# Kernel tuning notes

Hardware: AMD Instinct MI355X
Metric: run time of the kernel (lower is better)

Reference implementation:

```python
import jax, jax.numpy as jnp
import numpy as np

B, L, C, H, W = 8, 8, 64, 56, 56
K = 3
EPS = 1e-5


def setup_inputs() -> dict:
    key = jax.random.key(0)
    ks = jax.random.split(key, 7)
    s = lambda k, shape, sc=0.05: jax.random.normal(k, shape, dtype=jnp.float32) * sc
    return {
        "x": jax.random.normal(ks[0], (B, L, C, H, W), dtype=jnp.float32),
        "temporal_w": s(ks[1], (C, C)),        # Conv3d 1x1x1 C->C
        "temporal_b": s(ks[2], (C,)),
        "fc_w": s(ks[3], (C,)),                # Conv3d 1x1x1 C->1
        "fc_b": s(ks[4], (1,)),
        "conv_w": s(ks[5], (C, C, K, K), 0.1), # self.weight [1,1,Co,Ci,k,k] core
        "conv_b": s(ks[6], (C,)),              # self.bias [1,1,Co] core
        "bn_gamma": jnp.ones((C,), jnp.float32),
        "bn_beta": jnp.zeros((C,), jnp.float32),
    }


def reference(x, temporal_w, temporal_b, fc_w, fc_b, conv_w, conv_b, bn_gamma, bn_beta):
    b, l, c, h, w = x.shape
    # ---- generateweight_fourier ----
    xin = jnp.transpose(x, (0, 2, 1, 3, 4))                # [B,C,L,H,W]
    f = jnp.fft.fft2(xin, axes=(3, 4), norm='ortho')       # spatial FFT
    f = jnp.fft.fft(f, axis=2, norm='ortho')               # temporal FFT
    allxin = xin + 0.01 * jnp.abs(f) * xin                 # Fourier2 attention + residual
    pooled = allxin.mean(axis=(3, 4))                      # AdaptiveAvgPool3d((None,1,1)) -> [B,C,L]
    # temporalconv: 1x1x1 Conv3d C->C on [B,C,L,1,1]
    calib = jnp.einsum('oc,bcl->bol', temporal_w, pooled) + temporal_b[None, :, None]  # [B,C,L]
    # fc: 1x1x1 Conv3d C->1
    fcout = jnp.einsum('c,bcl->bl', fc_w, pooled) + fc_b[0]                            # [B,L]
    # finalweight: weight[1,1,Co,Ci,k,k] * (calib+1) broadcast over Ci -> [B,L,Co,Ci,k,k]
    calib_blc = jnp.transpose(calib, (0, 2, 1)) + 1.0      # [B,L,Ci]
    fw = conv_w[None, None] * calib_blc[:, :, None, :, None, None]
    fb = conv_b[None, None, :] * (fcout + 1.0)[:, :, None] # [B,L,Co]
    # ---- dynamic per-(sample,frame) conv2d (groups = b*l) ----
    x_flat = x.reshape(b * l, c, h, w)
    fw_flat = fw.reshape(b * l, c, c, K, K)
    fb_flat = fb.reshape(b * l, c)

    def per_sample(xi, wi):
        return jax.lax.conv_general_dilated(
            xi[None], wi, window_strides=(1, 1), padding=[(1, 1), (1, 1)],
            dimension_numbers=('NCHW', 'OIHW', 'NCHW'))[0]

    out = jax.vmap(per_sample)(x_flat, fw_flat) + fb_flat[:, :, None, None]
    out = x_flat + out                                     # residual (gate=False)
    # BatchNorm2d (training-mode batch statistics)
    mean = out.mean(axis=(0, 2, 3), keepdims=True)
    var = out.var(axis=(0, 2, 3), keepdims=True)
    out = (out - mean) * jax.lax.rsqrt(var + EPS)
    out = out * bn_gamma[None, :, None, None] + bn_beta[None, :, None, None]
    out = out * jax.nn.sigmoid(out)                        # SiLU
    return out.reshape(b, l, c, h, w)
```

## Files before the change

kernel.cpp:

```cpp
#include <hip/hip_runtime.h>
#include <cmath>

#define HW 3136
#define NF 64
#define NBLK2 448

typedef __attribute__((ext_vector_type(8))) short short8;
typedef __attribute__((ext_vector_type(4))) float float4a;

__device__ __forceinline__ unsigned short f2bf(float f) {
    unsigned int u = __float_as_uint(f);
    u += 0x7fffu + ((u >> 16) & 1u);
    return (unsigned short)(u >> 16);
}
__device__ __forceinline__ float bf2f(unsigned short u) {
    return __uint_as_float(((unsigned int)u) << 16);
}

__global__ __launch_bounds__(256)
void pack_kernel(const float* __restrict__ cw,
                 unsigned short* __restrict__ Ffix,
                 unsigned short* __restrict__ Wp) {
    if (blockIdx.x < 64) {
        int idx = blockIdx.x * 256 + threadIdx.x;
        int j    = idx & 7;
        int lane = (idx >> 3) & 63;
        int ks   = (idx >> 9) & 3;
        int t    = (idx >> 11) & 3;
        int p    = (idx >> 13) & 1;
        int mn = t * 16 + (lane & 15);
        int k  = ks * 32 + (lane >> 4) * 8 + j;
        float val = 0.f;
        if (mn < 56 && k < 112) {
            int kk = (k < 56) ? k : k - 56;
            int prod = (mn * kk) % 56;
            float ang = -6.2831853071795864f * (float)prod / 56.0f;
            float cr = cosf(ang);
            float ci = sinf(ang);
            float first  = (p == 0) ? cr : ci;
            float second = (p == 0) ? -ci : cr;
            val = (k < 56) ? first : second;
        }
        Ffix[idx] = f2bf(val);
    } else {
        int idx = (blockIdx.x - 64) * 256 + threadIdx.x;
        if (idx < 36864) {
            int i  = idx & 63;
            int o  = (idx >> 6) & 63;
            int kk = idx >> 12;
            Wp[idx] = f2bf(cw[(o * 64 + i) * 9 + kk]);
        }
    }
}

__global__ __launch_bounds__(256, 2)
void fft_mfma_kernel(const float* __restrict__ x,
                     const unsigned short* __restrict__ Ffix,
                     float* __restrict__ pooled) {
    const int bc = blockIdx.x;
    const int c  = bc & 63;
    const int b  = bc >> 6;
    const int tid  = threadIdx.x;
    const int lane = tid & 63;
    const int wv   = tid >> 6;
    const int n    = lane & 15;
    const int q    = lane >> 4;

    __shared__ unsigned short sh[40352];
    unsigned short* xbf = sh;
    unsigned short* Tb  = sh + 25088;
    unsigned short* Ub  = sh + 25088 + 56 * 136;
    float* red = (float*)(sh + 40320);

    for (int t = tid; t < 7616; t += 256)
        ((unsigned int*)(sh + 25088))[t] = 0u;

    for (int t = tid; t < 6272; t += 256) {
        int l = t / 784, r = t - l * 784;
        float4 v = *(const float4*)(x + ((size_t)((b * 8 + l) * 64 + c)) * HW + r * 4);
        ushort4 o;
        o.x = f2bf(v.x); o.y = f2bf(v.y); o.z = f2bf(v.z); o.w = f2bf(v.w);
        *(ushort4*)(xbf + l * 3136 + r * 4) = o;
    }
    __syncthreads();

    #pragma unroll 1
    for (int lp = 0; lp < 5; ++lp) {
        float tr[8], ti[8];
        #pragma unroll
        for (int l = 0; l < 8; ++l) {
            float ang = -0.78539816339744831f * (float)((l * lp) & 7);
            tr[l] = cosf(ang);
            ti[l] = sinf(ang);
        }
        for (int s = tid; s < 784; s += 256) {
            int h = s / 14, w4 = s - h * 14;
            float re[4] = {0.f, 0.f, 0.f, 0.f}, im[4] = {0.f, 0.f, 0.f, 0.f};
            #pragma unroll
            for (int l = 0; l < 8; ++l) {
                ushort4 u = *(const ushort4*)(xbf + l * 3136 + h * 56 + w4 * 4);
                float v0 = bf2f(u.x), v1 = bf2f(u.y), v2 = bf2f(u.z), v3 = bf2f(u.w);
                re[0] += v0 * tr[l]; im[0] += v0 * ti[l];
                re[1] += v1 * tr[l]; im[1] += v1 * ti[l];
                re[2] += v2 * tr[l]; im[2] += v2 * ti[l];
                re[3] += v3 * tr[l]; im[3] += v3 * ti[l];
            }
            #pragma unroll
            for (int j = 0; j < 4; ++j) {
                int w = w4 * 4 + j;
                Tb[w * 136 + h]      = f2bf(re[j]);
                Tb[w * 136 + 56 + h] = f2bf(im[j]);
            }
        }
        __syncthreads();

        {
            const int p  = wv >> 1;
            const int mh = (wv & 1) * 2;
            float4a s1[2][4];
            #pragma unroll
            for (int mi = 0; mi < 2; ++mi)
                #pragma unroll
                for (int nt = 0; nt < 4; ++nt) s1[mi][nt] = (float4a){0.f, 0.f, 0.f, 0.f};
            #pragma unroll
            for (int ks = 0; ks < 4; ++ks) {
                short8 bfr[4];
                #pragma unroll
                for (int nt = 0; nt < 4; ++nt) {
                    int row = nt * 16 + n; if (row > 55) row = 55;
                    bfr[nt] = *(const short8*)(Tb + row * 136 + ks * 32 + q * 8);
                }
                #pragma unroll
                for (int mi = 0; mi < 2; ++mi) {
                    short8 afr = *(const short8*)(Ffix + ((((p * 4 + mh + mi) * 4 + ks) * 64 + lane) * 8));
                    #pragma unroll
                    for (int nt = 0; nt < 4; ++nt)
                        s1[mi][nt] = __builtin_amdgcn_mfma_f32_16x16x32_bf16(afr, bfr[nt], s1[mi][nt], 0, 0, 0);
                }
            }
            #pragma unroll
            for (int mi = 0; mi < 2; ++mi)
                #pragma unroll
                for (int nt = 0; nt < 4; ++nt)
                    #pragma unroll
                    for (int r = 0; r < 4; ++r) {
                        int kh = (mh + mi) * 16 + q * 4 + r;
                        int w  = nt * 16 + n;
                        if (kh < 56 && w < 56)
                            Ub[kh * 136 + p * 56 + w] = f2bf(s1[mi][nt][r]);
                    }
        }
        __syncthreads();

        const int mt = wv;
        short8 afr2[4];
        #pragma unroll
        for (int ks = 0; ks < 4; ++ks) {
            int row = mt * 16 + n; if (row > 55) row = 55;
            afr2[ks] = *(const short8*)(Ub + row * 136 + ks * 32 + q * 8);
        }
        float4a g[2][4];
        #pragma unroll
        for (int pp = 0; pp < 2; ++pp)
            #pragma unroll
            for (int nt = 0; nt < 4; ++nt) g[pp][nt] = (float4a){0.f, 0.f, 0.f, 0.f};
        #pragma unroll
        for (int pp = 0; pp < 2; ++pp)
            #pragma unroll
            for (int ks = 0; ks < 4; ++ks)
                #pragma unroll
                for (int nt = 0; nt < 4; ++nt) {
                    short8 bfr = *(const short8*)(Ffix + ((((pp * 4 + nt) * 4 + ks) * 64 + lane) * 8));
                    g[pp][nt] = __builtin_amdgcn_mfma_f32_16x16x32_bf16(afr2[ks], bfr, g[pp][nt], 0, 0, 0);
                }

        const bool doflip = (lp >= 1 && lp <= 3);
        const unsigned short* x1 = xbf + lp * 3136;
        const unsigned short* x2 = xbf + ((8 - lp) & 7) * 3136;
        float S1 = 0.f, X1 = 0.f, S2 = 0.f, X2 = 0.f;
        #pragma unroll
        for (int nt = 0; nt < 4; ++nt) {
            int kw = nt * 16 + n;
            if (kw < 56) {
                int kwf = (56 - kw) % 56;
                #pragma unroll
                for (int r = 0; r < 4; ++r) {
                    int kh = mt * 16 + q * 4 + r;
                    if (kh < 56) {
                        float gr = g[0][nt][r], gi = g[1][nt][r];
                        float mag = sqrtf(gr * gr + gi * gi);
                        float v1 = bf2f(x1[kh * 56 + kw]);
                        S1 += mag * v1; X1 += v1;
                        if (doflip) {
                            int khf = (56 - kh) % 56;
                            float v2 = bf2f(x2[khf * 56 + kwf]);
                            S2 += mag * v2; X2 += v2;
                        }
                    }
                }
            }
        }
        #pragma unroll
        for (int m = 1; m < 64; m <<= 1) {
            S1 += __shfl_xor(S1, m);
            X1 += __shfl_xor(X1, m);
            S2 += __shfl_xor(S2, m);
            X2 += __shfl_xor(X2, m);
        }
        if (lane == 0) { red[wv * 4 + 0] = S1; red[wv * 4 + 1] = X1;
                         red[wv * 4 + 2] = S2; red[wv * 4 + 3] = X2; }
        __syncthreads();
        if (tid == 0) {
            float s1 = 0.f, xs1 = 0.f, s2 = 0.f, xs2 = 0.f;
            #pragma unroll
            for (int w = 0; w < 4; ++w) {
                s1 += red[w * 4 + 0]; xs1 += red[w * 4 + 1];
                s2 += red[w * 4 + 2]; xs2 += red[w * 4 + 3];
            }
            const float kS = 0.01f / (56.0f * 2.8284271247461903f);
            pooled[bc * 8 + lp] = (xs1 + kS * s1) / 3136.0f;
            if (doflip)
                pooled[bc * 8 + (8 - lp)] = (xs2 + kS * s2) / 3136.0f;
        }
    }
}

__global__ __launch_bounds__(64)
void calib_kernel(const float* __restrict__ pooled,
                  const float* __restrict__ tw_, const float* __restrict__ tb,
                  const float* __restrict__ fcw, const float* __restrict__ fcb,
                  const float* __restrict__ convb,
                  float* __restrict__ scale, float* __restrict__ fbias) {
    const int nn = blockIdx.x;
    const int b = nn >> 3, l = nn & 7;
    const int o = threadIdx.x;
    const float* pr = pooled + b * 512 + l;
    float dot = 0.f;
    #pragma unroll 8
    for (int c0 = 0; c0 < 64; ++c0) dot += tw_[o * 64 + c0] * pr[c0 * 8];
    float fcp = fcw[o] * pr[o * 8];
    #pragma unroll
    for (int off = 32; off > 0; off >>= 1) fcp += __shfl_down(fcp, off);
    float fcout = __shfl(fcp, 0) + fcb[0];
    scale[nn * 64 + o] = 1.0f + tb[o] + dot;
    fbias[nn * 64 + o] = convb[o] * (fcout + 1.0f);
}

__global__ __launch_bounds__(256, 2)
void conv_mfma_kernel(const float* __restrict__ x,
                      const unsigned short* __restrict__ Wp,
                      const float* __restrict__ scale, const float* __restrict__ fbias,
                      float* __restrict__ out,
                      float* __restrict__ psum, float* __restrict__ psum2) {
    const int rt = blockIdx.x;
    const int nn = blockIdx.y;
    const int tid  = threadIdx.x;
    const int lane = tid & 63;
    const int wv   = tid >> 6;
    const int r0   = rt * 8;

    __shared__ unsigned short xs[10 * 60 * 64];
    __shared__ float fb[64], ssc[64], rsc[64], bn1[64], bn2[64];

    if (tid < 64) {
        fb[tid]  = fbias[nn * 64 + tid];
        float s  = scale[nn * 64 + tid];
        ssc[tid] = s;
        rsc[tid] = 1.0f / s;
        bn1[tid] = 0.f; bn2[tid] = 0.f;
    }
    __syncthreads();

    for (int t = tid; t < 10240; t += 256) {
        if (t < 8960) {
            int c4 = t % 14;
            int rr = (t / 14) % 10;
            int i  = t / 140;
            int gr = r0 - 1 + rr;
            float4 v = make_float4(0.f, 0.f, 0.f, 0.f);
            if (gr >= 0 && gr < 56)
                v = *(const float4*)(x + ((size_t)(nn * 64 + i) * HW + gr * 56 + c4 * 4));
            float s = ssc[i];
            int g = i >> 3, il = i & 7;
            float vv[4] = {v.x, v.y, v.z, v.w};
            #pragma unroll
            for (int j = 0; j < 4; ++j) {
                int lc = c4 * 4 + 1 + j;
                xs[(rr * 60 + lc) * 64 + (((g ^ (lc & 7)) << 3) | il)] = f2bf(vv[j] * s);
            }
        } else {
            int idx = t - 8960;
            int i   = idx / 20;
            int rem = idx - i * 20;
            int rr  = rem >> 1;
            int lc  = (rem & 1) * 57;
            int g = i >> 3, il = i & 7;
            xs[(rr * 60 + lc) * 64 + (((g ^ (lc & 7)) << 3) | il)] = 0;
        }
    }
    __syncthreads();

    const int pxo = lane & 15;
    const int q   = lane >> 4;

    float4a acc[7][4];
    #pragma unroll
    for (int j = 0; j < 7; ++j)
        #pragma unroll
        for (int ot = 0; ot < 4; ++ot) acc[j][ot] = (float4a){0.f, 0.f, 0.f, 0.f};

    int rp[7], cp[7];
    #pragma unroll
    for (int j = 0; j < 7; ++j) {
        int px = (wv * 7 + j) * 16 + pxo;
        rp[j] = px / 56;
        cp[j] = px - rp[j] * 56;
    }

    #pragma unroll 1
    for (int kk = 0; kk < 9; ++kk) {
        const int dr = kk / 3, dc = kk - dr * 3;
        short8 a[4][2];
        #pragma unroll
        for (int ot = 0; ot < 4; ++ot)
            #pragma unroll
            for (int ih = 0; ih < 2; ++ih)
                a[ot][ih] = *(const short8*)(Wp + ((kk * 64 + ot * 16 + pxo) * 64 + ih * 32 + q * 8));

        #pragma unroll
        for (int j = 0; j < 7; ++j) {
            int lc = cp[j] + dc;
            int base = ((rp[j] + dr) * 60 + lc) * 64;
            int sw = lc & 7;
            #pragma unroll
            for (int ih = 0; ih < 2; ++ih) {
                short8 bv = *(const short8*)&xs[base + (((q + ih * 4) ^ sw) << 3)];
                #pragma unroll
                for (int ot = 0; ot < 4; ++ot)
                    acc[j][ot] = __builtin_amdgcn_mfma_f32_16x16x32_bf16(a[ot][ih], bv, acc[j][ot], 0, 0, 0);
            }
        }
    }

    float bs[4][4], bs2[4][4];
    #pragma unroll
    for (int ot = 0; ot < 4; ++ot)
        #pragma unroll
        for (int r = 0; r < 4; ++r) { bs[ot][r] = 0.f; bs2[ot][r] = 0.f; }

    #pragma unroll
    for (int j = 0; j < 7; ++j) {
        int px  = (wv * 7 + j) * 16 + pxo;
        int gpx = r0 * 56 + px;
        int rr  = rp[j] + 1;
        int lc  = cp[j] + 1;
        int sw  = lc & 7;
        int rowbase = (rr * 60 + lc) * 64;
        #pragma unroll
        for (int ot = 0; ot < 4; ++ot) {
            int g  = ot * 2 + (q >> 1);
            ushort4 uu = *(const ushort4*)(xs + rowbase + (((g ^ sw) << 3) | ((q & 1) * 4)));
            float resid[4] = {bf2f(uu.x), bf2f(uu.y), bf2f(uu.z), bf2f(uu.w)};
            #pragma unroll
            for (int r = 0; r < 4; ++r) {
                int o = ot * 16 + q * 4 + r;
                size_t off = (size_t)(nn * 64 + o) * HW + gpx;
                float v = acc[j][ot][r] + resid[r] * rsc[o] + fb[o];
                out[off] = v;
                bs[ot][r]  += v;
                bs2[ot][r] += v * v;
            }
        }
    }
    #pragma unroll
    for (int ot = 0; ot < 4; ++ot)
        #pragma unroll
        for (int r = 0; r < 4; ++r) {
            #pragma unroll
            for (int m = 1; m < 16; m <<= 1) {
                bs[ot][r]  += __shfl_xor(bs[ot][r], m);
                bs2[ot][r] += __shfl_xor(bs2[ot][r], m);
            }
        }
    if (pxo == 0) {
        #pragma unroll
        for (int ot = 0; ot < 4; ++ot)
            #pragma unroll
            for (int r = 0; r < 4; ++r) {
                int o = ot * 16 + q * 4 + r;
                atomicAdd(&bn1[o], bs[ot][r]);
                atomicAdd(&bn2[o], bs2[ot][r]);
            }
    }
    __syncthreads();
    if (tid < 64) {
        int bl = nn * 7 + rt;
        psum[bl * 64 + tid]  = bn1[tid];
        psum2[bl * 64 + tid] = bn2[tid];
    }
}

__global__ __launch_bounds__(256)
void bnstat_kernel(const float* __restrict__ psum, const float* __restrict__ psum2,
                   float* __restrict__ bn) {
    const int o = blockIdx.x;
    const int tid = threadIdx.x;
    float s = 0.f, s2 = 0.f;
    for (int bl = tid; bl < NBLK2; bl += 256) {
        s  += psum[bl * 64 + o];
        s2 += psum2[bl * 64 + o];
    }
    __shared__ float r1[256], r2[256];
    r1[tid] = s; r2[tid] = s2;
    __syncthreads();
    for (int st = 128; st > 0; st >>= 1) {
        if (tid < st) { r1[tid] += r1[tid + st]; r2[tid] += r2[tid + st]; }
        __syncthreads();
    }
    if (tid == 0) {
        const float N = 64.0f * (float)HW;
        float mean = r1[0] / N;
        float var  = r2[0] / N - mean * mean;
        bn[o]      = mean;
        bn[64 + o] = rsqrtf(var + 1e-5f);
    }
}

__global__ __launch_bounds__(256)
void bnsilu_kernel(float* __restrict__ out, const float* __restrict__ bn,
                   const float* __restrict__ gamma, const float* __restrict__ beta) {
    size_t idx = (size_t)blockIdx.x * 256 + threadIdx.x;
    if (idx >= (size_t)NF * 64 * HW) return;
    int c = (int)((idx / HW) & 63);
    float v = out[idx];
    float y = (v - bn[c]) * bn[64 + c] * gamma[c] + beta[c];
    out[idx] = y / (1.0f + expf(-y));
}

extern "C" void kernel_launch(void* const* d_in, const int* in_sizes, int n_in,
                              void* d_out, int out_size, void* d_ws, size_t ws_size,
                              hipStream_t stream) {
    const float* x          = (const float*)d_in[0];
    const float* temporal_w = (const float*)d_in[1];
    const float* temporal_b = (const float*)d_in[2];
    const float* fc_w       = (const float*)d_in[3];
    const float* fc_b       = (const float*)d_in[4];
    const float* conv_w     = (const float*)d_in[5];
    const float* conv_b     = (const float*)d_in[6];
    const float* bn_gamma   = (const float*)d_in[7];
    const float* bn_beta    = (const float*)d_in[8];
    float* out = (float*)d_out;
    float* ws  = (float*)d_ws;

    float* pooled = ws;
    float* scale  = ws + 4096;
    float* fbias  = ws + 8192;
    unsigned short* Wp = (unsigned short*)(ws + 12288);
    float* psum   = ws + 12288 + 18432;
    float* psum2  = psum + NBLK2 * 64;
    float* bn     = psum2 + NBLK2 * 64;
    unsigned short* Ffix = (unsigned short*)(bn + 128);

    pack_kernel<<<208, 256, 0, stream>>>(conv_w, Ffix, Wp);
    fft_mfma_kernel<<<512, 256, 0, stream>>>(x, Ffix, pooled);
    calib_kernel<<<64, 64, 0, stream>>>(pooled, temporal_w, temporal_b,
                                        fc_w, fc_b, conv_b, scale, fbias);
    conv_mfma_kernel<<<dim3(7, 64), 256, 0, stream>>>(x, Wp, scale, fbias,
                                                      out, psum, psum2);
    bnstat_kernel<<<64, 256, 0, stream>>>(psum, psum2, bn);
    int total = NF * 64 * HW;
    bnsilu_kernel<<<(total + 255) / 256, 256, 0, stream>>>(out, bn, bn_gamma, bn_beta);
}
```

Before: 227.1 us.

## Split FFT pooling into temporal-DFT and per-frequency 2D-DFT kernels, halve conv row tiles

The fused per-(b,c) FFT kernel, which launched only 512 blocks, is split in two. A temporal-DFT kernel writes bf16 intermediates into the output buffer as scratch, and a 2D-DFT kernel then runs one block per (b,c,temporal frequency), giving 2560 blocks. The conv kernel processes 4 rows per block instead of 8, doubling the grid to 896 blocks with less shared memory and a higher occupancy hint. The aim is more parallelism and occupancy, at the cost of extra global traffic for the intermediates, more halo reloads in the conv, and more partial-sum rows for the BN stats.

```diff
diff --git a/kernel.cpp b/kernel.cpp
--- a/kernel.cpp
+++ b/kernel.cpp
@@ -3,7 +3,7 @@
 
 #define HW 3136
 #define NF 64
-#define NBLK2 448
+#define NBLK3 896
 
 typedef __attribute__((ext_vector_type(8))) short short8;
 typedef __attribute__((ext_vector_type(4))) float float4a;
@@ -16,6 +16,9 @@
 __device__ __forceinline__ float bf2f(unsigned short u) {
     return __uint_as_float(((unsigned int)u) << 16);
 }
+
+__device__ __constant__ float TW8C[8] = {1.f, 0.70710678f, 0.f, -0.70710678f, -1.f, -0.70710678f, 0.f, 0.70710678f};
+__device__ __constant__ float TW8S[8] = {0.f, -0.70710678f, -1.f, -0.70710678f, 0.f, 0.70710678f, 1.f, 0.70710678f};
 
 __global__ __launch_bounds__(256)
 void pack_kernel(const float* __restrict__ cw,
@@ -53,175 +56,186 @@
     }
 }
 
-__global__ __launch_bounds__(256, 2)
-void fft_mfma_kernel(const float* __restrict__ x,
-                     const unsigned short* __restrict__ Ffix,
-                     float* __restrict__ pooled) {
-    const int bc = blockIdx.x;
-    const int c  = bc & 63;
-    const int b  = bc >> 6;
+__global__ __launch_bounds__(256)
+void tdft_kernel(const float* __restrict__ x, unsigned short* __restrict__ Tg) {
+    const int chunk = blockIdx.x & 1;
+    const int bc    = blockIdx.x >> 1;
+    const int c     = bc & 63;
+    const int b     = bc >> 6;
+    const int tid   = threadIdx.x;
+
+    const float* xb = x + ((size_t)(b * 512 + c)) * HW;
+
+    for (int g = chunk * 392 + tid; g < (chunk + 1) * 392; g += 256) {
+        float4 v[8];
+        #pragma unroll
+        for (int l = 0; l < 8; ++l)
+            v[l] = *(const float4*)(xb + (size_t)l * 64 * HW + g * 4);
+        #pragma unroll
+        for (int lp = 0; lp < 5; ++lp) {
+            float re[4] = {0.f, 0.f, 0.f, 0.f}, im[4] = {0.f, 0.f, 0.f, 0.f};
+            #pragma unroll
+            for (int l = 0; l < 8; ++l) {
+                float tr = TW8C[(l * lp) & 7], ti = TW8S[(l * lp) & 7];
+                re[0] += v[l].x * tr; im[0] += v[l].x * ti;
+                re[1] += v[l].y * tr; im[1] += v[l].y * ti;
+                re[2] += v[l].z * tr; im[2] += v[l].z * ti;
+                re[3] += v[l].w * tr; im[3] += v[l].w * ti;
+            }
+            ushort4 ur, ui;
+            ur.x = f2bf(re[0]); ur.y = f2bf(re[1]); ur.z = f2bf(re[2]); ur.w = f2bf(re[3]);
+            ui.x = f2bf(im[0]); ui.y = f2bf(im[1]); ui.z = f2bf(im[2]); ui.w = f2bf(im[3]);
+            size_t base = ((size_t)(bc * 5 + lp) * 2) * HW + g * 4;
+            *(ushort4*)(Tg + base)      = ur;
+            *(ushort4*)(Tg + base + HW) = ui;
+        }
+    }
+}
+
+__global__ __launch_bounds__(256)
+void fft2_kernel(const float* __restrict__ x,
+                 const unsigned short* __restrict__ Tg,
+                 const unsigned short* __restrict__ Ffix,
+                 float* __restrict__ pooled) {
+    const int bid = blockIdx.x;
+    const int lp  = bid % 5;
+    const int bc  = bid / 5;
+    const int c   = bc & 63;
+    const int b   = bc >> 6;
     const int tid  = threadIdx.x;
     const int lane = tid & 63;
     const int wv   = tid >> 6;
     const int n    = lane & 15;
     const int q    = lane >> 4;
 
-    __shared__ unsigned short sh[40352];
-    unsigned short* xbf = sh;
-    unsigned short* Tb  = sh + 25088;
-    unsigned short* Ub  = sh + 25088 + 56 * 136;
-    float* red = (float*)(sh + 40320);
-
-    for (int t = tid; t < 7616; t += 256)
-        ((unsigned int*)(sh + 25088))[t] = 0u;
-
-    for (int t = tid; t < 6272; t += 256) {
-        int l = t / 784, r = t - l * 784;
-        float4 v = *(const float4*)(x + ((size_t)((b * 8 + l) * 64 + c)) * HW + r * 4);
-        ushort4 o;
-        o.x = f2bf(v.x); o.y = f2bf(v.y); o.z = f2bf(v.z); o.w = f2bf(v.w);
-        *(ushort4*)(xbf + l * 3136 + r * 4) = o;
-    }
-    __syncthreads();
-
-    #pragma unroll 1
-    for (int lp = 0; lp < 5; ++lp) {
-        float tr[8], ti[8];
-        #pragma unroll
-        for (int l = 0; l < 8; ++l) {
-            float ang = -0.78539816339744831f * (float)((l * lp) & 7);
-            tr[l] = cosf(ang);
-            ti[l] = sinf(ang);
-        }
-        for (int s = tid; s < 784; s += 256) {
-            int h = s / 14, w4 = s - h * 14;
-            float re[4] = {0.f, 0.f, 0.f, 0.f}, im[4] = {0.f, 0.f, 0.f, 0.f};
-            #pragma unroll
-            for (int l = 0; l < 8; ++l) {
-                ushort4 u = *(const ushort4*)(xbf + l * 3136 + h * 56 + w4 * 4);
-                float v0 = bf2f(u.x), v1 = bf2f(u.y), v2 = bf2f(u.z), v3 = bf2f(u.w);
-                re[0] += v0 * tr[l]; im[0] += v0 * ti[l];
-                re[1] += v1 * tr[l]; im[1] += v1 * ti[l];
-                re[2] += v2 * tr[l]; im[2] += v2 * ti[l];
-                re[3] += v3 * tr[l]; im[3] += v3 * ti[l];
-            }
-            #pragma unroll
-            for (int j = 0; j < 4; ++j) {
-                int w = w4 * 4 + j;
-                Tb[w * 136 + h]      = f2bf(re[j]);
-                Tb[w * 136 + 56 + h] = f2bf(im[j]);
-            }
-        }
-        __syncthreads();
-
-        {
-            const int p  = wv >> 1;
-            const int mh = (wv & 1) * 2;
-            float4a s1[2][4];
-            #pragma unroll
-            for (int mi = 0; mi < 2; ++mi)
-                #pragma unroll
-                for (int nt = 0; nt < 4; ++nt) s1[mi][nt] = (float4a){0.f, 0.f, 0.f, 0.f};
-            #pragma unroll
-            for (int ks = 0; ks < 4; ++ks) {
-                short8 bfr[4];
-                #pragma unroll
-                for (int nt = 0; nt < 4; ++nt) {
-                    int row = nt * 16 + n; if (row > 55) row = 55;
-                    bfr[nt] = *(const short8*)(Tb + row * 136 + ks * 32 + q * 8);
-                }
-                #pragma unroll
-                for (int mi = 0; mi < 2; ++mi) {
-                    short8 afr = *(const short8*)(Ffix + ((((p * 4 + mh + mi) * 4 + ks) * 64 + lane) * 8));
-                    #pragma unroll
-                    for (int nt = 0; nt < 4; ++nt)
-                        s1[mi][nt] = __builtin_amdgcn_mfma_f32_16x16x32_bf16(afr, bfr[nt], s1[mi][nt], 0, 0, 0);
-                }
-            }
-            #pragma unroll
-            for (int mi = 0; mi < 2; ++mi)
+    __shared__ unsigned short Tb[56 * 136];
+    __shared__ unsigned short Ub[56 * 136];
+    __shared__ float red[16];
+
+    for (int t = tid; t < 1344; t += 256) {
+        int row = t / 24, k = 112 + t % 24;
+        Tb[row * 136 + k] = 0;
+        Ub[row * 136 + k] = 0;
+    }
+    const unsigned short* tg = Tg + (size_t)bid * 2 * HW;
+    for (int t = tid; t < 1568; t += 256) {
+        int ri = t / 784, g = t - ri * 784;
+        ushort4 u = *(const ushort4*)(tg + ri * HW + g * 4);
+        int h = g / 14, w4 = g - h * 14;
+        Tb[(w4 * 4 + 0) * 136 + ri * 56 + h] = u.x;
+        Tb[(w4 * 4 + 1) * 136 + ri * 56 + h] = u.y;
+        Tb[(w4 * 4 + 2) * 136 + ri * 56 + h] = u.z;
+        Tb[(w4 * 4 + 3) * 136 + ri * 56 + h] = u.w;
+    }
+    __syncthreads();
+
+    {
+        const int p  = wv >> 1;
+        const int mh = (wv & 1) * 2;
+        float4a s1[2][4];
+        #pragma unroll
+        for (int mi = 0; mi < 2; ++mi)
+            #pragma unroll
+            for (int nt = 0; nt < 4; ++nt) s1[mi][nt] = (float4a){0.f, 0.f, 0.f, 0.f};
+        #pragma unroll
+        for (int ks = 0; ks < 4; ++ks) {
+            short8 bfr[4];
+            #pragma unroll
+            for (int nt = 0; nt < 4; ++nt) {
+                int row = nt * 16 + n; if (row > 55) row = 55;
+                bfr[nt] = *(const short8*)(Tb + row * 136 + ks * 32 + q * 8);
+            }
+            #pragma unroll
+            for (int mi = 0; mi < 2; ++mi) {
+                short8 afr = *(const short8*)(Ffix + ((((p * 4 + mh + mi) * 4 + ks) * 64 + lane) * 8));
                 #pragma unroll
                 for (int nt = 0; nt < 4; ++nt)
-                    #pragma unroll
-                    for (int r = 0; r < 4; ++r) {
-                        int kh = (mh + mi) * 16 + q * 4 + r;
-                        int w  = nt * 16 + n;
-                        if (kh < 56 && w < 56)
-                            Ub[kh * 136 + p * 56 + w] = f2bf(s1[mi][nt][r]);
-                    }
-        }
-        __syncthreads();
-
-        const int mt = wv;
-        short8 afr2[4];
-        #pragma unroll
-        for (int ks = 0; ks < 4; ++ks) {
-            int row = mt * 16 + n; if (row > 55) row = 55;
-            afr2[ks] = *(const short8*)(Ub + row * 136 + ks * 32 + q * 8);
-        }
-        float4a g[2][4];
-        #pragma unroll
-        for (int pp = 0; pp < 2; ++pp)
-            #pragma unroll
-            for (int nt = 0; nt < 4; ++nt) g[pp][nt] = (float4a){0.f, 0.f, 0.f, 0.f};
-        #pragma unroll
-        for (int pp = 0; pp < 2; ++pp)
-            #pragma unroll
-            for (int ks = 0; ks < 4; ++ks)
-                #pragma unroll
-                for (int nt = 0; nt < 4; ++nt) {
-                    short8 bfr = *(const short8*)(Ffix + ((((pp * 4 + nt) * 4 + ks) * 64 + lane) * 8));
-                    g[pp][nt] = __builtin_amdgcn_mfma_f32_16x16x32_bf16(afr2[ks], bfr, g[pp][nt], 0, 0, 0);
-                }
-
-        const bool doflip = (lp >= 1 && lp <= 3);
-        const unsigned short* x1 = xbf + lp * 3136;
-        const unsigned short* x2 = xbf + ((8 - lp) & 7) * 3136;
-        float S1 = 0.f, X1 = 0.f, S2 = 0.f, X2 = 0.f;
-        #pragma unroll
-        for (int nt = 0; nt < 4; ++nt) {
-            int kw = nt * 16 + n;
-            if (kw < 56) {
-                int kwf = (56 - kw) % 56;
+                    s1[mi][nt] = __builtin_amdgcn_mfma_f32_16x16x32_bf16(afr, bfr[nt], s1[mi][nt], 0, 0, 0);
+            }
+        }
+        #pragma unroll
+        for (int mi = 0; mi < 2; ++mi)
+            #pragma unroll
+            for (int nt = 0; nt < 4; ++nt)
                 #pragma unroll
                 for (int r = 0; r < 4; ++r) {
-                    int kh = mt * 16 + q * 4 + r;
-                    if (kh < 56) {
-                        float gr = g[0][nt][r], gi = g[1][nt][r];
-                        float mag = sqrtf(gr * gr + gi * gi);
-                        float v1 = bf2f(x1[kh * 56 + kw]);
-                        S1 += mag * v1; X1 += v1;
-                        if (doflip) {
-                            int khf = (56 - kh) % 56;
-                            float v2 = bf2f(x2[khf * 56 + kwf]);
-                            S2 += mag * v2; X2 += v2;
-                        }
+                    int kh = (mh + mi) * 16 + q * 4 + r;
+                    int w  = nt * 16 + n;
+                    if (kh < 56 && w < 56)
+                        Ub[kh * 136 + p * 56 + w] = f2bf(s1[mi][nt][r]);
+                }
+    }
+    __syncthreads();
+
+    const int mt = wv;
+    short8 afr2[4];
+    #pragma unroll
+    for (int ks = 0; ks < 4; ++ks) {
+        int row = mt * 16 + n; if (row > 55) row = 55;
+        afr2[ks] = *(const short8*)(Ub + row * 136 + ks * 32 + q * 8);
+    }
+    float4a g[2][4];
+    #pragma unroll
+    for (int pp = 0; pp < 2; ++pp)
+        #pragma unroll
+        for (int nt = 0; nt < 4; ++nt) g[pp][nt] = (float4a){0.f, 0.f, 0.f, 0.f};
+    #pragma unroll
+    for (int pp = 0; pp < 2; ++pp)
+        #pragma unroll
+        for (int ks = 0; ks < 4; ++ks)
+            #pragma unroll
+            for (int nt = 0; nt < 4; ++nt) {
+                short8 bfr = *(const short8*)(Ffix + ((((pp * 4 + nt) * 4 + ks) * 64 + lane) * 8));
+                g[pp][nt] = __builtin_amdgcn_mfma_f32_16x16x32_bf16(afr2[ks], bfr, g[pp][nt], 0, 0, 0);
+            }
+
+    const bool doflip = (lp >= 1 && lp <= 3);
+    const float* x1 = x + ((size_t)((b * 8 + lp) * 64 + c)) * HW;
+    const float* x2 = x + ((size_t)((b * 8 + ((8 - lp) & 7)) * 64 + c)) * HW;
+    float S1 = 0.f, X1 = 0.f, S2 = 0.f, X2 = 0.f;
+    #pragma unroll
+    for (int nt = 0; nt < 4; ++nt) {
+        int kw = nt * 16 + n;
+        if (kw < 56) {
+            int kwf = (56 - kw) % 56;
+            #pragma unroll
+            for (int r = 0; r < 4; ++r) {
+                int kh = mt * 16 + q * 4 + r;
+                if (kh < 56) {
+                    float gr = g[0][nt][r], gi = g[1][nt][r];
+                    float mag = sqrtf(gr * gr + gi * gi);
+                    float v1 = x1[kh * 56 + kw];
+                    S1 += mag * v1; X1 += v1;
+                    if (doflip) {
+                        int khf = (56 - kh) % 56;
+                        float v2 = x2[khf * 56 + kwf];
+                        S2 += mag * v2; X2 += v2;
                     }
                 }
             }
         }
-        #pragma unroll
-        for (int m = 1; m < 64; m <<= 1) {
-            S1 += __shfl_xor(S1, m);
-            X1 += __shfl_xor(X1, m);
-            S2 += __shfl_xor(S2, m);
-            X2 += __shfl_xor(X2, m);
-        }
-        if (lane == 0) { red[wv * 4 + 0] = S1; red[wv * 4 + 1] = X1;
-                         red[wv * 4 + 2] = S2; red[wv * 4 + 3] = X2; }
-        __syncthreads();
-        if (tid == 0) {
-            float s1 = 0.f, xs1 = 0.f, s2 = 0.f, xs2 = 0.f;
-            #pragma unroll
-            for (int w = 0; w < 4; ++w) {
-                s1 += red[w * 4 + 0]; xs1 += red[w * 4 + 1];
-                s2 += red[w * 4 + 2]; xs2 += red[w * 4 + 3];
-            }
-            const float kS = 0.01f / (56.0f * 2.8284271247461903f);
-            pooled[bc * 8 + lp] = (xs1 + kS * s1) / 3136.0f;
-            if (doflip)
-                pooled[bc * 8 + (8 - lp)] = (xs2 + kS * s2) / 3136.0f;
-        }
+    }
+    #pragma unroll
+    for (int m = 1; m < 64; m <<= 1) {
+        S1 += __shfl_xor(S1, m);
+        X1 += __shfl_xor(X1, m);
+        S2 += __shfl_xor(S2, m);
+        X2 += __shfl_xor(X2, m);
+    }
+    if (lane == 0) { red[wv * 4 + 0] = S1; red[wv * 4 + 1] = X1;
+                     red[wv * 4 + 2] = S2; red[wv * 4 + 3] = X2; }
+    __syncthreads();
+    if (tid == 0) {
+        float s1 = 0.f, xs1 = 0.f, s2 = 0.f, xs2 = 0.f;
+        #pragma unroll
+        for (int w = 0; w < 4; ++w) {
+            s1 += red[w * 4 + 0]; xs1 += red[w * 4 + 1];
+            s2 += red[w * 4 + 2]; xs2 += red[w * 4 + 3];
+        }
+        const float kS = 0.01f / (56.0f * 2.8284271247461903f);
+        pooled[bc * 8 + lp] = (xs1 + kS * s1) / 3136.0f;
+        if (doflip)
+            pooled[bc * 8 + (8 - lp)] = (xs2 + kS * s2) / 3136.0f;
     }
 }
 
@@ -246,7 +260,7 @@
     fbias[nn * 64 + o] = convb[o] * (fcout + 1.0f);
 }
 
-__global__ __launch_bounds__(256, 2)
+__global__ __launch_bounds__(256, 3)
 void conv_mfma_kernel(const float* __restrict__ x,
                       const unsigned short* __restrict__ Wp,
                       const float* __restrict__ scale, const float* __restrict__ fbias,
@@ -257,9 +271,9 @@
     const int tid  = threadIdx.x;
     const int lane = tid & 63;
     const int wv   = tid >> 6;
-    const int r0   = rt * 8;
-
-    __shared__ unsigned short xs[10 * 60 * 64];
+    const int r0   = rt * 4;
+
+    __shared__ unsigned short xs[6 * 60 * 64];
     __shared__ float fb[64], ssc[64], rsc[64], bn1[64], bn2[64];
 
     if (tid < 64) {
@@ -271,31 +285,31 @@
     }
     __syncthreads();
 
-    for (int t = tid; t < 10240; t += 256) {
-        if (t < 8960) {
+    for (int t = tid; t < 6144; t += 256) {
+        if (t < 5376) {
             int c4 = t % 14;
-            int rr = (t / 14) % 10;
-            int i  = t / 140;
+            int rr = (t / 14) % 6;
+            int i  = t / 84;
             int gr = r0 - 1 + rr;
             float4 v = make_float4(0.f, 0.f, 0.f, 0.f);
             if (gr >= 0 && gr < 56)
                 v = *(const float4*)(x + ((size_t)(nn * 64 + i) * HW + gr * 56 + c4 * 4));
             float s = ssc[i];
-            int g = i >> 3, il = i & 7;
+            int gg = i >> 3, il = i & 7;
             float vv[4] = {v.x, v.y, v.z, v.w};
             #pragma unroll
             for (int j = 0; j < 4; ++j) {
                 int lc = c4 * 4 + 1 + j;
-                xs[(rr * 60 + lc) * 64 + (((g ^ (lc & 7)) << 3) | il)] = f2bf(vv[j] * s);
+                xs[(rr * 60 + lc) * 64 + (((gg ^ (lc & 7)) << 3) | il)] = f2bf(vv[j] * s);
             }
         } else {
-            int idx = t - 8960;
-            int i   = idx / 20;
-            int rem = idx - i * 20;
+            int idx = t - 5376;
+            int i   = idx / 12;
+            int rem = idx - i * 12;
             int rr  = rem >> 1;
             int lc  = (rem & 1) * 57;
-            int g = i >> 3, il = i & 7;
-            xs[(rr * 60 + lc) * 64 + (((g ^ (lc & 7)) << 3) | il)] = 0;
+            int gg = i >> 3, il = i & 7;
+            xs[(rr * 60 + lc) * 64 + (((gg ^ (lc & 7)) << 3) | il)] = 0;
         }
     }
     __syncthreads();
@@ -303,16 +317,20 @@
     const int pxo = lane & 15;
     const int q   = lane >> 4;
 
-    float4a acc[7][4];
-    #pragma unroll
-    for (int j = 0; j < 7; ++j)
+    float4a acc[4][4];
+    #pragma unroll
+    for (int j = 0; j < 4; ++j)
         #pragma unroll
         for (int ot = 0; ot < 4; ++ot) acc[j][ot] = (float4a){0.f, 0.f, 0.f, 0.f};
 
-    int rp[7], cp[7];
-    #pragma unroll
-    for (int j = 0; j < 7; ++j) {
-        int px = (wv * 7 + j) * 16 + pxo;
+    int rp[4], cp[4];
+    bool vld[4];
+    #pragma unroll
+    for (int j = 0; j < 4; ++j) {
+        int tl = wv + 4 * j;
+        vld[j] = (tl < 14);
+        if (tl > 13) tl = 13;
+        int px = tl * 16 + pxo;
         rp[j] = px / 56;
         cp[j] = px - rp[j] * 56;
     }
@@ -328,7 +346,7 @@
                 a[ot][ih] = *(const short8*)(Wp + ((kk * 64 + ot * 16 + pxo) * 64 + ih * 32 + q * 8));
 
         #pragma unroll
-        for (int j = 0; j < 7; ++j) {
+        for (int j = 0; j < 4; ++j) {
             int lc = cp[j] + dc;
             int base = ((rp[j] + dr) * 60 + lc) * 64;
             int sw = lc & 7;
@@ -349,8 +367,9 @@
         for (int r = 0; r < 4; ++r) { bs[ot][r] = 0.f; bs2[ot][r] = 0.f; }
 
     #pragma unroll
-    for (int j = 0; j < 7; ++j) {
-        int px  = (wv * 7 + j) * 16 + pxo;
+    for (int j = 0; j < 4; ++j) {
+        if (!vld[j]) continue;
+        int px  = (wv + 4 * j) * 16 + pxo;
         int gpx = r0 * 56 + px;
         int rr  = rp[j] + 1;
         int lc  = cp[j] + 1;
@@ -358,8 +377,8 @@
         int rowbase = (rr * 60 + lc) * 64;
         #pragma unroll
         for (int ot = 0; ot < 4; ++ot) {
-            int g  = ot * 2 + (q >> 1);
-            ushort4 uu = *(const ushort4*)(xs + rowbase + (((g ^ sw) << 3) | ((q & 1) * 4)));
+            int gg = ot * 2 + (q >> 1);
+            ushort4 uu = *(const ushort4*)(xs + rowbase + (((gg ^ sw) << 3) | ((q & 1) * 4)));
             float resid[4] = {bf2f(uu.x), bf2f(uu.y), bf2f(uu.z), bf2f(uu.w)};
             #pragma unroll
             for (int r = 0; r < 4; ++r) {
@@ -394,7 +413,7 @@
     }
     __syncthreads();
     if (tid < 64) {
-        int bl = nn * 7 + rt;
+        int bl = nn * 14 + rt;
         psum[bl * 64 + tid]  = bn1[tid];
         psum2[bl * 64 + tid] = bn2[tid];
     }
@@ -406,7 +425,7 @@
     const int o = blockIdx.x;
     const int tid = threadIdx.x;
     float s = 0.f, s2 = 0.f;
-    for (int bl = tid; bl < NBLK2; bl += 256) {
+    for (int bl = tid; bl < NBLK3; bl += 256) {
         s  += psum[bl * 64 + o];
         s2 += psum2[bl * 64 + o];
     }
@@ -457,16 +476,19 @@
     float* fbias  = ws + 8192;
     unsigned short* Wp = (unsigned short*)(ws + 12288);
     float* psum   = ws + 12288 + 18432;
-    float* psum2  = psum + NBLK2 * 64;
-    float* bn     = psum2 + NBLK2 * 64;
+    float* psum2  = psum + NBLK3 * 64;
+    float* bn     = psum2 + NBLK3 * 64;
     unsigned short* Ffix = (unsigned short*)(bn + 128);
 
+    unsigned short* Tg = (unsigned short*)d_out;
+
     pack_kernel<<<208, 256, 0, stream>>>(conv_w, Ffix, Wp);
-    fft_mfma_kernel<<<512, 256, 0, stream>>>(x, Ffix, pooled);
+    tdft_kernel<<<1024, 256, 0, stream>>>(x, Tg);
+    fft2_kernel<<<2560, 256, 0, stream>>>(x, Tg, Ffix, pooled);
     calib_kernel<<<64, 64, 0, stream>>>(pooled, temporal_w, temporal_b,
                                         fc_w, fc_b, conv_b, scale, fbias);
-    conv_mfma_kernel<<<dim3(7, 64), 256, 0, stream>>>(x, Wp, scale, fbias,
-                                                      out, psum, psum2);
+    conv_mfma_kernel<<<dim3(14, 64), 256, 0, stream>>>(x, Wp, scale, fbias,
+                                                       out, psum, psum2);
     bnstat_kernel<<<64, 256, 0, stream>>>(psum, psum2, bn);
     int total = NF * 64 * HW;
     bnsilu_kernel<<<(total + 255) / 256, 256, 0, stream>>>(out, bn, bn_gamma, bn_beta);
```

Result: slower. 260.9 us (+14.9%).

## Split Fourier pooling into temporal-DFT and batched spatial-DFT kernels

Applied to the files above, without the earlier changes.

The single FFT kernel, which looped over five temporal frequencies per (b,c) block, is replaced by two kernels. The first computes the 8-point temporal DFT straight from fp32 input using constant twiddles and writes bf16 real/imag planes into the output buffer as scratch. The second runs one block per (b, frequency, channel pair) and batches two channels into the MFMA N dimension, giving 1280 blocks instead of 512. This exposes more parallelism and removes the serial per-frequency loop, at the cost of an extra global write/read of the intermediate spectrum and extra fp32 input reads for the weighting.

```diff
diff --git a/kernel.cpp b/kernel.cpp
--- a/kernel.cpp
+++ b/kernel.cpp
@@ -16,6 +16,9 @@
 __device__ __forceinline__ float bf2f(unsigned short u) {
     return __uint_as_float(((unsigned int)u) << 16);
 }
+
+__device__ __constant__ float TW8C[8] = {1.f, 0.70710678f, 0.f, -0.70710678f, -1.f, -0.70710678f, 0.f, 0.70710678f};
+__device__ __constant__ float TW8S[8] = {0.f, -0.70710678f, -1.f, -0.70710678f, 0.f, 0.70710678f, 1.f, 0.70710678f};
 
 __global__ __launch_bounds__(256)
 void pack_kernel(const float* __restrict__ cw,
@@ -53,175 +56,196 @@
     }
 }
 
-__global__ __launch_bounds__(256, 2)
-void fft_mfma_kernel(const float* __restrict__ x,
-                     const unsigned short* __restrict__ Ffix,
-                     float* __restrict__ pooled) {
-    const int bc = blockIdx.x;
-    const int c  = bc & 63;
-    const int b  = bc >> 6;
+__global__ __launch_bounds__(256)
+void tdft_kernel(const float* __restrict__ x, unsigned short* __restrict__ Tg) {
+    const int chunk = blockIdx.x & 1;
+    const int bc    = blockIdx.x >> 1;
+    const int c     = bc & 63;
+    const int b     = bc >> 6;
+    const int tid   = threadIdx.x;
+
+    const float* xb = x + ((size_t)(b * 512 + c)) * HW;
+
+    for (int g = chunk * 392 + tid; g < (chunk + 1) * 392; g += 256) {
+        float4 v[8];
+        #pragma unroll
+        for (int l = 0; l < 8; ++l)
+            v[l] = *(const float4*)(xb + (size_t)l * 64 * HW + g * 4);
+        #pragma unroll
+        for (int lp = 0; lp < 5; ++lp) {
+            float re[4] = {0.f, 0.f, 0.f, 0.f}, im[4] = {0.f, 0.f, 0.f, 0.f};
+            #pragma unroll
+            for (int l = 0; l < 8; ++l) {
+                float tr = TW8C[(l * lp) & 7], ti = TW8S[(l * lp) & 7];
+                re[0] += v[l].x * tr; im[0] += v[l].x * ti;
+                re[1] += v[l].y * tr; im[1] += v[l].y * ti;
+                re[2] += v[l].z * tr; im[2] += v[l].z * ti;
+                re[3] += v[l].w * tr; im[3] += v[l].w * ti;
+            }
+            ushort4 ur, ui;
+            ur.x = f2bf(re[0]); ur.y = f2bf(re[1]); ur.z = f2bf(re[2]); ur.w = f2bf(re[3]);
+            ui.x = f2bf(im[0]); ui.y = f2bf(im[1]); ui.z = f2bf(im[2]); ui.w = f2bf(im[3]);
+            size_t base = ((size_t)(bc * 5 + lp) * 2) * HW + g * 4;
+            *(ushort4*)(Tg + base)      = ur;
+            *(ushort4*)(Tg + base + HW) = ui;
+        }
+    }
+}
+
+__global__ __launch_bounds__(256)
+void fft2b_kernel(const float* __restrict__ x,
+                  const unsigned short* __restrict__ Tg,
+                  const unsigned short* __restrict__ Ffix,
+                  float* __restrict__ pooled) {
+    const int bid = blockIdx.x;
+    const int ch  = bid & 31;
+    const int rem = bid >> 5;
+    const int lp  = rem % 5;
+    const int b   = rem / 5;
+    const int c0  = ch * 2;
     const int tid  = threadIdx.x;
     const int lane = tid & 63;
     const int wv   = tid >> 6;
-    const int n    = lane & 15;
+    const int n16  = lane & 15;
     const int q    = lane >> 4;
 
-    __shared__ unsigned short sh[40352];
-    unsigned short* xbf = sh;
-    unsigned short* Tb  = sh + 25088;
-    unsigned short* Ub  = sh + 25088 + 56 * 136;
-    float* red = (float*)(sh + 40320);
-
-    for (int t = tid; t < 7616; t += 256)
-        ((unsigned int*)(sh + 25088))[t] = 0u;
-
-    for (int t = tid; t < 6272; t += 256) {
-        int l = t / 784, r = t - l * 784;
-        float4 v = *(const float4*)(x + ((size_t)((b * 8 + l) * 64 + c)) * HW + r * 4);
-        ushort4 o;
-        o.x = f2bf(v.x); o.y = f2bf(v.y); o.z = f2bf(v.z); o.w = f2bf(v.w);
-        *(ushort4*)(xbf + l * 3136 + r * 4) = o;
-    }
-    __syncthreads();
-
-    #pragma unroll 1
-    for (int lp = 0; lp < 5; ++lp) {
-        float tr[8], ti[8];
-        #pragma unroll
-        for (int l = 0; l < 8; ++l) {
-            float ang = -0.78539816339744831f * (float)((l * lp) & 7);
-            tr[l] = cosf(ang);
-            ti[l] = sinf(ang);
-        }
-        for (int s = tid; s < 784; s += 256) {
-            int h = s / 14, w4 = s - h * 14;
-            float re[4] = {0.f, 0.f, 0.f, 0.f}, im[4] = {0.f, 0.f, 0.f, 0.f};
-            #pragma unroll
-            for (int l = 0; l < 8; ++l) {
-                ushort4 u = *(const ushort4*)(xbf + l * 3136 + h * 56 + w4 * 4);
-                float v0 = bf2f(u.x), v1 = bf2f(u.y), v2 = bf2f(u.z), v3 = bf2f(u.w);
-                re[0] += v0 * tr[l]; im[0] += v0 * ti[l];
-                re[1] += v1 * tr[l]; im[1] += v1 * ti[l];
-                re[2] += v2 * tr[l]; im[2] += v2 * ti[l];
-                re[3] += v3 * tr[l]; im[3] += v3 * ti[l];
-            }
-            #pragma unroll
-            for (int j = 0; j < 4; ++j) {
-                int w = w4 * 4 + j;
-                Tb[w * 136 + h]      = f2bf(re[j]);
-                Tb[w * 136 + 56 + h] = f2bf(im[j]);
-            }
-        }
-        __syncthreads();
-
-        {
-            const int p  = wv >> 1;
-            const int mh = (wv & 1) * 2;
-            float4a s1[2][4];
-            #pragma unroll
-            for (int mi = 0; mi < 2; ++mi)
-                #pragma unroll
-                for (int nt = 0; nt < 4; ++nt) s1[mi][nt] = (float4a){0.f, 0.f, 0.f, 0.f};
-            #pragma unroll
-            for (int ks = 0; ks < 4; ++ks) {
-                short8 bfr[4];
-                #pragma unroll
-                for (int nt = 0; nt < 4; ++nt) {
-                    int row = nt * 16 + n; if (row > 55) row = 55;
-                    bfr[nt] = *(const short8*)(Tb + row * 136 + ks * 32 + q * 8);
+    __shared__ unsigned short AB[112 * 136];
+    __shared__ float pacc[2][4];
+
+    if (tid < 8) ((float*)pacc)[tid] = 0.f;
+    for (int t = tid; t < 1344; t += 256) {
+        int row = t / 12, kk2 = t - row * 12;
+        *(unsigned int*)&AB[row * 136 + 112 + kk2 * 2] = 0u;
+    }
+    for (int t = tid; t < 3136; t += 256) {
+        int ci = t / 1568;
+        int r2 = t - ci * 1568;
+        int ri = r2 / 784, g = r2 - ri * 784;
+        size_t plane = ((size_t)((b * 64 + c0 + ci) * 5 + lp) * 2 + ri) * HW;
+        ushort4 u = *(const ushort4*)(Tg + plane + g * 4);
+        int h = g / 14, w4 = g - h * 14;
+        int base = (ci * 56 + w4 * 4) * 136 + ri * 56 + h;
+        AB[base]           = u.x;
+        AB[base + 136]     = u.y;
+        AB[base + 272]     = u.z;
+        AB[base + 408]     = u.w;
+    }
+    __syncthreads();
+
+    const int p   = wv >> 1;
+    const int mh2 = (wv & 1) * 2;
+    float4a s1[2][7];
+    #pragma unroll
+    for (int mi = 0; mi < 2; ++mi)
+        #pragma unroll
+        for (int nt = 0; nt < 7; ++nt) s1[mi][nt] = (float4a){0.f, 0.f, 0.f, 0.f};
+    #pragma unroll
+    for (int ks = 0; ks < 4; ++ks) {
+        short8 bfr[7];
+        #pragma unroll
+        for (int nt = 0; nt < 7; ++nt)
+            bfr[nt] = *(const short8*)&AB[(nt * 16 + n16) * 136 + ks * 32 + q * 8];
+        #pragma unroll
+        for (int mi = 0; mi < 2; ++mi) {
+            short8 afr = *(const short8*)(Ffix + ((((p * 4 + mh2 + mi) * 4 + ks) * 64 + lane) * 8));
+            #pragma unroll
+            for (int nt = 0; nt < 7; ++nt)
+                s1[mi][nt] = __builtin_amdgcn_mfma_f32_16x16x32_bf16(afr, bfr[nt], s1[mi][nt], 0, 0, 0);
+        }
+    }
+    __syncthreads();
+
+    #pragma unroll
+    for (int mi = 0; mi < 2; ++mi)
+        #pragma unroll
+        for (int nt = 0; nt < 7; ++nt)
+            #pragma unroll
+            for (int r = 0; r < 4; ++r) {
+                int kh = (mh2 + mi) * 16 + q * 4 + r;
+                if (kh < 56) {
+                    int nidx = nt * 16 + n16;
+                    int ci = (nidx >= 56) ? 1 : 0;
+                    int w  = nidx - ci * 56;
+                    AB[(ci * 56 + kh) * 136 + p * 56 + w] = f2bf(s1[mi][nt][r]);
                 }
-                #pragma unroll
-                for (int mi = 0; mi < 2; ++mi) {
-                    short8 afr = *(const short8*)(Ffix + ((((p * 4 + mh + mi) * 4 + ks) * 64 + lane) * 8));
-                    #pragma unroll
-                    for (int nt = 0; nt < 4; ++nt)
-                        s1[mi][nt] = __builtin_amdgcn_mfma_f32_16x16x32_bf16(afr, bfr[nt], s1[mi][nt], 0, 0, 0);
-                }
-            }
-            #pragma unroll
-            for (int mi = 0; mi < 2; ++mi)
-                #pragma unroll
-                for (int nt = 0; nt < 4; ++nt)
-                    #pragma unroll
-                    for (int r = 0; r < 4; ++r) {
-                        int kh = (mh + mi) * 16 + q * 4 + r;
-                        int w  = nt * 16 + n;
-                        if (kh < 56 && w < 56)
-                            Ub[kh * 136 + p * 56 + w] = f2bf(s1[mi][nt][r]);
-                    }
-        }
-        __syncthreads();
-
-        const int mt = wv;
+            }
+    __syncthreads();
+
+    const bool doflip = (lp >= 1 && lp <= 3);
+    const float* x1a = x + ((size_t)((b * 8 + lp) * 64 + c0)) * HW;
+    const float* x1b = x1a + HW;
+    const float* x2a = x + ((size_t)((b * 8 + ((8 - lp) & 7)) * 64 + c0)) * HW;
+    const float* x2b = x2a + HW;
+    float Sa = 0.f, Xa = 0.f, Sb = 0.f, Xb = 0.f;
+    float S2a = 0.f, X2a = 0.f, S2b = 0.f, X2b = 0.f;
+
+    #pragma unroll
+    for (int ui = 0; ui < 2; ++ui) {
+        int mt2 = wv + ui * 4;
+        if (mt2 > 6) continue;
         short8 afr2[4];
         #pragma unroll
-        for (int ks = 0; ks < 4; ++ks) {
-            int row = mt * 16 + n; if (row > 55) row = 55;
-            afr2[ks] = *(const short8*)(Ub + row * 136 + ks * 32 + q * 8);
-        }
-        float4a g[2][4];
-        #pragma unroll
-        for (int pp = 0; pp < 2; ++pp)
-            #pragma unroll
-            for (int nt = 0; nt < 4; ++nt) g[pp][nt] = (float4a){0.f, 0.f, 0.f, 0.f};
-        #pragma unroll
-        for (int pp = 0; pp < 2; ++pp)
-            #pragma unroll
-            for (int ks = 0; ks < 4; ++ks)
-                #pragma unroll
-                for (int nt = 0; nt < 4; ++nt) {
-                    short8 bfr = *(const short8*)(Ffix + ((((pp * 4 + nt) * 4 + ks) * 64 + lane) * 8));
-                    g[pp][nt] = __builtin_amdgcn_mfma_f32_16x16x32_bf16(afr2[ks], bfr, g[pp][nt], 0, 0, 0);
-                }
-
-        const bool doflip = (lp >= 1 && lp <= 3);
-        const unsigned short* x1 = xbf + lp * 3136;
-        const unsigned short* x2 = xbf + ((8 - lp) & 7) * 3136;
-        float S1 = 0.f, X1 = 0.f, S2 = 0.f, X2 = 0.f;
+        for (int ks = 0; ks < 4; ++ks)
+            afr2[ks] = *(const short8*)&AB[(mt2 * 16 + n16) * 136 + ks * 32 + q * 8];
+        float4a gr[4], gi[4];
+        #pragma unroll
+        for (int nt = 0; nt < 4; ++nt) { gr[nt] = (float4a){0.f,0.f,0.f,0.f}; gi[nt] = (float4a){0.f,0.f,0.f,0.f}; }
+        #pragma unroll
+        for (int ks = 0; ks < 4; ++ks)
+            #pragma unroll
+            for (int nt = 0; nt < 4; ++nt) {
+                short8 b0 = *(const short8*)(Ffix + (((nt * 4 + ks) * 64 + lane) * 8));
+                short8 b1 = *(const short8*)(Ffix + ((((4 + nt) * 4 + ks) * 64 + lane) * 8));
+                gr[nt] = __builtin_amdgcn_mfma_f32_16x16x32_bf16(afr2[ks], b0, gr[nt], 0, 0, 0);
+                gi[nt] = __builtin_amdgcn_mfma_f32_16x16x32_bf16(afr2[ks], b1, gi[nt], 0, 0, 0);
+            }
         #pragma unroll
         for (int nt = 0; nt < 4; ++nt) {
-            int kw = nt * 16 + n;
+            int kw = nt * 16 + n16;
             if (kw < 56) {
                 int kwf = (56 - kw) % 56;
                 #pragma unroll
                 for (int r = 0; r < 4; ++r) {
-                    int kh = mt * 16 + q * 4 + r;
-                    if (kh < 56) {
-                        float gr = g[0][nt][r], gi = g[1][nt][r];
-                        float mag = sqrtf(gr * gr + gi * gi);
-                        float v1 = bf2f(x1[kh * 56 + kw]);
-                        S1 += mag * v1; X1 += v1;
-                        if (doflip) {
-                            int khf = (56 - kh) % 56;
-                            float v2 = bf2f(x2[khf * 56 + kwf]);
-                            S2 += mag * v2; X2 += v2;
-                        }
+                    int m  = mt2 * 16 + q * 4 + r;
+                    int ci = (m >= 56) ? 1 : 0;
+                    int kh = m - ci * 56;
+                    float grv = gr[nt][r], giv = gi[nt][r];
+                    float mag = sqrtf(grv * grv + giv * giv);
+                    const float* xp1 = ci ? x1b : x1a;
+                    float v1 = xp1[kh * 56 + kw];
+                    if (ci) { Sb += mag * v1; Xb += v1; }
+                    else    { Sa += mag * v1; Xa += v1; }
+                    if (doflip) {
+                        int khf = (56 - kh) % 56;
+                        const float* xp2 = ci ? x2b : x2a;
+                        float v2 = xp2[khf * 56 + kwf];
+                        if (ci) { S2b += mag * v2; X2b += v2; }
+                        else    { S2a += mag * v2; X2a += v2; }
                     }
                 }
             }
         }
-        #pragma unroll
-        for (int m = 1; m < 64; m <<= 1) {
-            S1 += __shfl_xor(S1, m);
-            X1 += __shfl_xor(X1, m);
-            S2 += __shfl_xor(S2, m);
-            X2 += __shfl_xor(X2, m);
-        }
-        if (lane == 0) { red[wv * 4 + 0] = S1; red[wv * 4 + 1] = X1;
-                         red[wv * 4 + 2] = S2; red[wv * 4 + 3] = X2; }
-        __syncthreads();
-        if (tid == 0) {
-            float s1 = 0.f, xs1 = 0.f, s2 = 0.f, xs2 = 0.f;
-            #pragma unroll
-            for (int w = 0; w < 4; ++w) {
-                s1 += red[w * 4 + 0]; xs1 += red[w * 4 + 1];
-                s2 += red[w * 4 + 2]; xs2 += red[w * 4 + 3];
-            }
-            const float kS = 0.01f / (56.0f * 2.8284271247461903f);
-            pooled[bc * 8 + lp] = (xs1 + kS * s1) / 3136.0f;
-            if (doflip)
-                pooled[bc * 8 + (8 - lp)] = (xs2 + kS * s2) / 3136.0f;
-        }
+    }
+    #pragma unroll
+    for (int m = 1; m < 64; m <<= 1) {
+        Sa += __shfl_xor(Sa, m);   Xa += __shfl_xor(Xa, m);
+        Sb += __shfl_xor(Sb, m);   Xb += __shfl_xor(Xb, m);
+        S2a += __shfl_xor(S2a, m); X2a += __shfl_xor(X2a, m);
+        S2b += __shfl_xor(S2b, m); X2b += __shfl_xor(X2b, m);
+    }
+    if (lane == 0) {
+        atomicAdd(&pacc[0][0], Sa);  atomicAdd(&pacc[0][1], Xa);
+        atomicAdd(&pacc[1][0], Sb);  atomicAdd(&pacc[1][1], Xb);
+        atomicAdd(&pacc[0][2], S2a); atomicAdd(&pacc[0][3], X2a);
+        atomicAdd(&pacc[1][2], S2b); atomicAdd(&pacc[1][3], X2b);
+    }
+    __syncthreads();
+    if (tid < 2) {
+        const float kS = 0.01f / (56.0f * 2.8284271247461903f);
+        int c = c0 + tid;
+        pooled[(b * 64 + c) * 8 + lp] = (pacc[tid][1] + kS * pacc[tid][0]) / 3136.0f;
+        if (doflip)
+            pooled[(b * 64 + c) * 8 + (8 - lp)] = (pacc[tid][3] + kS * pacc[tid][2]) / 3136.0f;
     }
 }
 
@@ -461,8 +485,11 @@
     float* bn     = psum2 + NBLK2 * 64;
     unsigned short* Ffix = (unsigned short*)(bn + 128);
 
+    unsigned short* Tg = (unsigned short*)d_out;
+
     pack_kernel<<<208, 256, 0, stream>>>(conv_w, Ffix, Wp);
-    fft_mfma_kernel<<<512, 256, 0, stream>>>(x, Ffix, pooled);
+    tdft_kernel<<<1024, 256, 0, stream>>>(x, Tg);
+    fft2b_kernel<<<1280, 256, 0, stream>>>(x, Tg, Ffix, pooled);
     calib_kernel<<<64, 64, 0, stream>>>(pooled, temporal_w, temporal_b,
                                         fc_w, fc_b, conv_b, scale, fbias);
     conv_mfma_kernel<<<dim3(7, 64), 256, 0, stream>>>(x, Wp, scale, fbias,
```

New measurement: 240.7 us. 6.0% more time.
